# Optimization experiments

Measured on AMD Instinct MI355X. Metric: run time of the kernel, lower is better.

Reference implementation:

```python
import jax, jax.numpy as jnp
import numpy as np

FS = 4  # filter_size: input3 has FS*FS channels (DAIN default)


def setup_inputs() -> dict:
    key = jax.random.key(0)
    k1, k2, k3 = jax.random.split(key, 3)
    B, C, H, W = 4, 3, 544, 960
    input1 = jax.random.normal(k1, (B, C, H, W), jnp.float32)          # image
    input2 = jax.random.normal(k2, (B, 2, H, W), jnp.float32)          # flow (x, y)
    input3 = jax.random.uniform(k3, (B, FS * FS, H, W), jnp.float32)   # per-pixel filters
    return {"input1": input1, "input2": input2, "input3": input3}


def _filter_interp(input1, input2, input3):
    B, C, H, W = input1.shape
    fs = int(round(np.sqrt(input3.shape[1])))
    fx = input2[:, 0]  # [B,H,W]
    fy = input2[:, 1]
    xs = jnp.arange(W, dtype=input1.dtype)
    ys = jnp.arange(H, dtype=input1.dtype)
    x2 = xs[None, None, :] + fx   # sample x position per output pixel
    y2 = ys[None, :, None] + fy
    mask = ((x2 >= 0) & (y2 >= 0) & (x2 <= W - 1) & (y2 <= H - 1)
            & (jnp.abs(fx) < W / 2.0) & (jnp.abs(fy) < H / 2.0))
    x2c = jnp.clip(x2, 0.0, W - 1)
    y2c = jnp.clip(y2, 0.0, H - 1)
    ix = jnp.floor(x2c).astype(jnp.int32)   # int(x2), x2>=0 inside mask
    iy = jnp.floor(y2c).astype(jnp.int32)
    alpha = (x2c - ix).astype(input1.dtype)  # fractional part
    beta = (y2c - iy).astype(input1.dtype)
    ixL = ix + 1 - fs // 2                   # top-left tap of filter window
    iyT = iy + 1 - fs // 2

    img = input1.reshape(B, C, H * W)

    def gather(yi, xi):
        # yi, xi: int [B,H,W] (already clamped) -> [B,C,H,W]
        idx = (yi * W + xi).reshape(B, 1, H * W)
        g = jnp.take_along_axis(img, jnp.broadcast_to(idx, (B, C, H * W)), axis=2)
        return g.reshape(B, C, H, W)

    # bilinear blend weights of the four shifted window sums (TL,TR,BL,BR)
    wa = ((1 - alpha) * (1 - beta))[:, None]
    wb = (alpha * (1 - beta))[:, None]
    wc = ((1 - alpha) * beta)[:, None]
    wd = (alpha * beta)[:, None]

    out = jnp.zeros_like(input1)
    for j in range(fs):          # fixed small filter window, unrolled
        yT = jnp.clip(iyT + j, 0, H - 1)
        yB = jnp.clip(iyT + j + 1, 0, H - 1)
        for i in range(fs):
            xL = jnp.clip(ixL + i, 0, W - 1)
            xR = jnp.clip(ixL + i + 1, 0, W - 1)
            samp = (wa * gather(yT, xL) + wb * gather(yT, xR)
                    + wc * gather(yB, xL) + wd * gather(yB, xR))
            out = out + samp * input3[:, j * fs + i][:, None]
    return out * mask[:, None].astype(input1.dtype)


def reference(input1, input2, input3):
    return _filter_interp(input1, input2, input3)
```

## Files before the change

kernel.cpp:

```cpp
#include <hip/hip_runtime.h>


#define BB 4
#define HH 544
#define WW 960
#define HW (HH * WW)

#define BX 64
#define BY 8
#define MARG 6
#define TW (BX + 2 * MARG)
#define TH (BY + 2 * MARG)
#define TSW (TW * 3 + 1)

typedef float v2f __attribute__((ext_vector_type(2)));

__global__ __launch_bounds__(256) void filt_interp_kernel(
    const float* __restrict__ img,
    const float* __restrict__ flow,
    const float* __restrict__ filt,
    float* __restrict__ out)
{
    __shared__ float tile[TH * TSW];

    const int tid = threadIdx.x;
    const int x0 = blockIdx.x * BX;
    const int y0 = blockIdx.y * BY;
    const int b  = blockIdx.z;
    const int tx0 = x0 - MARG;
    const int ty0 = y0 - MARG;

    const float* ibase = img + (size_t)b * 3 * HW;
    for (int li = tid; li < TH * TW; li += 256) {
        int vr = li / TW;
        int vc = li - vr * TW;
        int gy = min(max(ty0 + vr, 0), HH - 1);
        int gx = min(max(tx0 + vc, 0), WW - 1);
        const float* ip = ibase + gy * WW + gx;
        float* tp = tile + vr * TSW + vc * 3;
        tp[0] = ip[0];
        tp[1] = ip[HW];
        tp[2] = ip[2 * HW];
    }
    __syncthreads();

    const int xp = tid & 31;
    const int yr = tid >> 5;
    const int x = x0 + 2 * xp;
    const int y = y0 + yr;
    const int pix = y * WW + x;

    v2f fxp = __builtin_nontemporal_load((const v2f*)(flow + (size_t)(b * 2 + 0) * HW + pix));
    v2f fyp = __builtin_nontemporal_load((const v2f*)(flow + (size_t)(b * 2 + 1) * HW + pix));
    const float* fp = filt + (size_t)b * 16 * HW + pix;
    v2f w3p[16];
#pragma unroll
    for (int t = 0; t < 16; t++)
        w3p[t] = __builtin_nontemporal_load((const v2f*)(fp + (size_t)t * HW));

    float res[2][3];

#pragma unroll
    for (int k = 0; k < 2; k++) {
        const int xk = x + k;
        float fx = fxp[k];
        float fy = fyp[k];
        float x2 = (float)xk + fx;
        float y2 = (float)y + fy;
        bool m = (x2 >= 0.0f) && (y2 >= 0.0f) &&
                 (x2 <= (float)(WW - 1)) && (y2 <= (float)(HH - 1)) &&
                 (fabsf(fx) < (float)WW * 0.5f) && (fabsf(fy) < (float)HH * 0.5f);
        float x2c = fminf(fmaxf(x2, 0.0f), (float)(WW - 1));
        float y2c = fminf(fmaxf(y2, 0.0f), (float)(HH - 1));
        int ix = (int)floorf(x2c);
        int iy = (int)floorf(y2c);
        float alpha = x2c - (float)ix;
        float beta  = y2c - (float)iy;
        int ixL = ix - 1;
        int iyT = iy - 1;
        float mf = m ? 1.0f : 0.0f;
        float wa = (1.0f - alpha) * (1.0f - beta) * mf;
        float wb = alpha * (1.0f - beta) * mf;
        float wc = (1.0f - alpha) * beta * mf;
        float wd = alpha * beta * mf;

        float W5[5][5];
#pragma unroll
        for (int r = 0; r < 5; r++)
#pragma unroll
            for (int c = 0; c < 5; c++) W5[r][c] = 0.0f;

#pragma unroll
        for (int j = 0; j < 4; j++) {
#pragma unroll
            for (int i = 0; i < 4; i++) {
                float w3 = w3p[j * 4 + i][k];
                W5[j][i]         += wa * w3;
                W5[j][i + 1]     += wb * w3;
                W5[j + 1][i]     += wc * w3;
                W5[j + 1][i + 1] += wd * w3;
            }
        }

        float ax = 0.0f, ay = 0.0f, az = 0.0f;

        bool ok = (iyT >= ty0) && (iyT + 4 <= ty0 + TH - 1) &&
                  (ixL >= tx0) && (ixL + 4 <= tx0 + TW - 1);

        if (ok) {
            int base = (iyT - ty0) * TSW + (ixL - tx0) * 3;
#pragma unroll
            for (int r = 0; r < 5; r++) {
#pragma unroll
                for (int c = 0; c < 5; c++) {
                    const float* tp = tile + base + r * TSW + c * 3;
                    float w = W5[r][c];
                    ax = fmaf(w, tp[0], ax);
                    ay = fmaf(w, tp[1], ay);
                    az = fmaf(w, tp[2], az);
                }
            }
        } else {
            int cx[5], ry[5];
#pragma unroll
            for (int q = 0; q < 5; q++) {
                cx[q] = min(max(ixL + q, 0), WW - 1);
                ry[q] = min(max(iyT + q, 0), HH - 1);
            }
#pragma unroll
            for (int r = 0; r < 5; r++) {
                const float* rowp = ibase + ry[r] * WW;
#pragma unroll
                for (int c = 0; c < 5; c++) {
                    float w = W5[r][c];
                    const float* p = rowp + cx[c];
                    ax = fmaf(w, p[0], ax);
                    ay = fmaf(w, p[HW], ay);
                    az = fmaf(w, p[2 * HW], az);
                }
            }
        }

        res[k][0] = ax;
        res[k][1] = ay;
        res[k][2] = az;
    }

    float* ob = out + (size_t)b * 3 * HW + pix;
    v2f s0 = {res[0][0], res[1][0]};
    v2f s1 = {res[0][1], res[1][1]};
    v2f s2 = {res[0][2], res[1][2]};
    __builtin_nontemporal_store(s0, (v2f*)(ob));
    __builtin_nontemporal_store(s1, (v2f*)(ob + HW));
    __builtin_nontemporal_store(s2, (v2f*)(ob + 2 * HW));
}

extern "C" void kernel_launch(void* const* d_in, const int* in_sizes, int n_in,
                              void* d_out, int out_size, void* d_ws, size_t ws_size,
                              hipStream_t stream) {
    const float* img  = (const float*)d_in[0];
    const float* flow = (const float*)d_in[1];
    const float* filt = (const float*)d_in[2];
    float* out = (float*)d_out;

    dim3 grid(WW / BX, HH / BY, BB);
    filt_interp_kernel<<<grid, 256, 0, stream>>>(img, flow, filt, out);
}
```

Before: 221.5 us.

## Store image tile as padded float4 and map pixels with stride-32 per thread

The shared image tile changes from interleaved 3-float entries to a padded float4 per pixel, so each tap becomes one 128-bit LDS read with vector FMA accumulation. Each thread now handles pixels x and x+32 instead of two adjacent pixels, so global loads and stores become scalar but fully coalesced across the wave, and neighbouring lanes hit neighbouring tile entries. The cost is a third more shared memory and more scalar global memory instructions in place of 64-bit vector ones.

```diff
diff --git a/kernel.cpp b/kernel.cpp
--- a/kernel.cpp
+++ b/kernel.cpp
@@ -11,9 +11,9 @@
 #define MARG 6
 #define TW (BX + 2 * MARG)
 #define TH (BY + 2 * MARG)
-#define TSW (TW * 3 + 1)
+#define RS4 (TW + 1)
 
-typedef float v2f __attribute__((ext_vector_type(2)));
+typedef float v4f __attribute__((ext_vector_type(4)));
 
 __global__ __launch_bounds__(256) void filt_interp_kernel(
     const float* __restrict__ img,
@@ -21,7 +21,7 @@
     const float* __restrict__ filt,
     float* __restrict__ out)
 {
-    __shared__ float tile[TH * TSW];
+    __shared__ v4f tile[TH * RS4];
 
     const int tid = threadIdx.x;
     const int x0 = blockIdx.x * BX;
@@ -37,34 +37,43 @@
         int gy = min(max(ty0 + vr, 0), HH - 1);
         int gx = min(max(tx0 + vc, 0), WW - 1);
         const float* ip = ibase + gy * WW + gx;
-        float* tp = tile + vr * TSW + vc * 3;
-        tp[0] = ip[0];
-        tp[1] = ip[HW];
-        tp[2] = ip[2 * HW];
+        v4f t;
+        t.x = ip[0];
+        t.y = ip[HW];
+        t.z = ip[2 * HW];
+        t.w = 0.0f;
+        tile[vr * RS4 + vc] = t;
     }
     __syncthreads();
 
     const int xp = tid & 31;
     const int yr = tid >> 5;
-    const int x = x0 + 2 * xp;
+    const int xb = x0 + xp;
     const int y = y0 + yr;
-    const int pix = y * WW + x;
+    const int pix = y * WW + xb;
 
-    v2f fxp = __builtin_nontemporal_load((const v2f*)(flow + (size_t)(b * 2 + 0) * HW + pix));
-    v2f fyp = __builtin_nontemporal_load((const v2f*)(flow + (size_t)(b * 2 + 1) * HW + pix));
+    const float* flp = flow + (size_t)b * 2 * HW + pix;
+    float fxk[2], fyk[2];
+    fxk[0] = __builtin_nontemporal_load(flp);
+    fxk[1] = __builtin_nontemporal_load(flp + 32);
+    fyk[0] = __builtin_nontemporal_load(flp + HW);
+    fyk[1] = __builtin_nontemporal_load(flp + HW + 32);
+
     const float* fp = filt + (size_t)b * 16 * HW + pix;
-    v2f w3p[16];
+    float w3k[2][16];
 #pragma unroll
-    for (int t = 0; t < 16; t++)
-        w3p[t] = __builtin_nontemporal_load((const v2f*)(fp + (size_t)t * HW));
+    for (int t = 0; t < 16; t++) {
+        w3k[0][t] = __builtin_nontemporal_load(fp + (size_t)t * HW);
+        w3k[1][t] = __builtin_nontemporal_load(fp + (size_t)t * HW + 32);
+    }
 
     float res[2][3];
 
 #pragma unroll
     for (int k = 0; k < 2; k++) {
-        const int xk = x + k;
-        float fx = fxp[k];
-        float fy = fyp[k];
+        const int xk = xb + 32 * k;
+        float fx = fxk[k];
+        float fy = fyk[k];
         float x2 = (float)xk + fx;
         float y2 = (float)y + fy;
         bool m = (x2 >= 0.0f) && (y2 >= 0.0f) &&
@@ -94,7 +103,7 @@
         for (int j = 0; j < 4; j++) {
 #pragma unroll
             for (int i = 0; i < 4; i++) {
-                float w3 = w3p[j * 4 + i][k];
+                float w3 = w3k[k][j * 4 + i];
                 W5[j][i]         += wa * w3;
                 W5[j][i + 1]     += wb * w3;
                 W5[j + 1][i]     += wc * w3;
@@ -102,25 +111,24 @@
             }
         }
 
-        float ax = 0.0f, ay = 0.0f, az = 0.0f;
-
         bool ok = (iyT >= ty0) && (iyT + 4 <= ty0 + TH - 1) &&
                   (ixL >= tx0) && (ixL + 4 <= tx0 + TW - 1);
 
         if (ok) {
-            int base = (iyT - ty0) * TSW + (ixL - tx0) * 3;
+            int base = (iyT - ty0) * RS4 + (ixL - tx0);
+            v4f acc = {0.0f, 0.0f, 0.0f, 0.0f};
 #pragma unroll
             for (int r = 0; r < 5; r++) {
 #pragma unroll
                 for (int c = 0; c < 5; c++) {
-                    const float* tp = tile + base + r * TSW + c * 3;
-                    float w = W5[r][c];
-                    ax = fmaf(w, tp[0], ax);
-                    ay = fmaf(w, tp[1], ay);
-                    az = fmaf(w, tp[2], az);
+                    acc += W5[r][c] * tile[base + r * RS4 + c];
                 }
             }
+            res[k][0] = acc.x;
+            res[k][1] = acc.y;
+            res[k][2] = acc.z;
         } else {
+            float ax = 0.0f, ay = 0.0f, az = 0.0f;
             int cx[5], ry[5];
 #pragma unroll
             for (int q = 0; q < 5; q++) {
@@ -139,20 +147,18 @@
                     az = fmaf(w, p[2 * HW], az);
                 }
             }
+            res[k][0] = ax;
+            res[k][1] = ay;
+            res[k][2] = az;
         }
-
-        res[k][0] = ax;
-        res[k][1] = ay;
-        res[k][2] = az;
     }
 
     float* ob = out + (size_t)b * 3 * HW + pix;
-    v2f s0 = {res[0][0], res[1][0]};
-    v2f s1 = {res[0][1], res[1][1]};
-    v2f s2 = {res[0][2], res[1][2]};
-    __builtin_nontemporal_store(s0, (v2f*)(ob));
-    __builtin_nontemporal_store(s1, (v2f*)(ob + HW));
-    __builtin_nontemporal_store(s2, (v2f*)(ob + 2 * HW));
+#pragma unroll
+    for (int ch = 0; ch < 3; ch++) {
+        __builtin_nontemporal_store(res[0][ch], ob + (size_t)ch * HW);
+        __builtin_nontemporal_store(res[1][ch], ob + (size_t)ch * HW + 32);
+    }
 }
 
 extern "C" void kernel_launch(void* const* d_in, const int* in_sizes, int n_in,
```

Result: no change. 218.6 us (-1.3%).
